# Kernel tuning notes

Measured on AMD Instinct MI355X. Metric: run time of the kernel, lower is better.

Reference implementation:

```python
import jax, jax.numpy as jnp
import numpy as np
from jax import lax

B, C, P, H = 4, 3, 160, 32          # batch of box patches, channels, patch size, score-net hidden
TEMB = 64                            # time-embedding dim
BETA0, BETA1 = 0.1, 20.0             # subVP SDE beta_min / beta_max
T_EPS = 1e-5                         # integration start time (timesteps=(1e-5, 1))
N_STEPS = 10                         # (1 - eps) / ode_step_size with step_size=0.1


def _conv(x, w, b):
    y = lax.conv_general_dilated(x, w, (1, 1), 'SAME',
                                 dimension_numbers=('NCHW', 'OIHW', 'NCHW'))
    return y + b[None, :, None, None]


def _time_emb(t):
    half = TEMB // 2
    freqs = jnp.exp(-np.log(10000.0) / (half - 1) * jnp.arange(half, dtype=jnp.float32))
    a = t[:, None] * 999.0 * freqs[None, :]   # continuous t scaled as in score_sde
    return jnp.concatenate([jnp.sin(a), jnp.cos(a)], axis=-1)


def _score_net(x, t, params):
    w1, b1, wt, bt, w2, b2, w3, b3 = params
    emb = _time_emb(t) @ wt + bt                       # [B, H]
    h = jax.nn.relu(_conv(x, w1, b1) + emb[:, :, None, None])
    h = jax.nn.relu(_conv(h, w2, b2))
    return _conv(h, w3, b3)


def _drift(x, tvec, params):
    # subVP probability-flow ODE drift: f(x,t) - 0.5 * g(t)^2 * score(x,t)
    bd = BETA1 - BETA0
    beta_t = BETA0 + tvec * bd
    lmc = -0.25 * tvec ** 2 * bd - 0.5 * tvec * BETA0   # log mean coeff
    std = 1.0 - jnp.exp(2.0 * lmc)                      # marginal std
    g2 = beta_t * (1.0 - jnp.exp(4.0 * lmc))            # diffusion^2
    score = _score_net(x, tvec, params) / std[:, None, None, None]
    return -0.5 * beta_t[:, None, None, None] * x - 0.5 * g2[:, None, None, None] * score


def _forward(patches, hs_epsilon, params):
    eps = jnp.broadcast_to(hs_epsilon, patches.shape)   # fixed Rademacher probe
    dt = (1.0 - T_EPS) / N_STEPS

    def rhs(x, t):
        tvec = jnp.ones((x.shape[0],), x.dtype) * t
        # Skilling-Hutchinson divergence: eps^T J eps via one jvp
        drift, jv = jax.jvp(lambda xx: _drift(xx, tvec, params), (x,), (eps,))
        return drift, jnp.sum(jv * eps, axis=(1, 2, 3))

    def step(carry, t0):
        x, lp = carry
        k1x, k1l = rhs(x, t0)
        k2x, k2l = rhs(x + 0.5 * dt * k1x, t0 + 0.5 * dt)
        k3x, k3l = rhs(x + 0.5 * dt * k2x, t0 + 0.5 * dt)
        k4x, k4l = rhs(x + dt * k3x, t0 + dt)
        x = x + (dt / 6.0) * (k1x + 2.0 * k2x + 2.0 * k3x + k4x)
        lp = lp + (dt / 6.0) * (k1l + 2.0 * k2l + 2.0 * k3l + k4l)
        return (x, lp), None

    ts = T_EPS + dt * jnp.arange(N_STEPS, dtype=patches.dtype)
    init = (patches, jnp.zeros((patches.shape[0],), patches.dtype))
    (z, delta_logp), _ = lax.scan(jax.checkpoint(step), init, ts)

    Ndim = float(np.prod(patches.shape[1:]))
    prior_logp = -0.5 * Ndim * np.log(2.0 * np.pi) - 0.5 * jnp.sum(z ** 2, axis=(1, 2, 3))
    bpd = -(prior_logp + delta_logp) / np.log(2.0)
    return bpd / Ndim                                   # per-patch NLL (bits/dim)


def setup_inputs() -> dict:
    key = jax.random.key(0)
    ks = jax.random.split(key, 6)
    s = 0.05
    return {
        'patches': jax.random.normal(ks[0], (B, C, P, P), jnp.float32),
        'hs_epsilon': jnp.sign(jax.random.normal(ks[1], (1, C, P, P), jnp.float32)),
        'w1': jax.random.normal(ks[2], (H, C, 3, 3), jnp.float32) * s,
        'b1': jnp.zeros((H,), jnp.float32),
        'wt': jax.random.normal(ks[3], (TEMB, H), jnp.float32) * s,
        'bt': jnp.zeros((H,), jnp.float32),
        'w2': jax.random.normal(ks[4], (H, H, 3, 3), jnp.float32) * s,
        'b2': jnp.zeros((H,), jnp.float32),
        'w3': jax.random.normal(ks[5], (C, H, 3, 3), jnp.float32) * s,
        'b3': jnp.zeros((C,), jnp.float32),
    }


def reference(patches, hs_epsilon, w1, b1, wt, bt, w2, b2, w3, b3):
    params = (w1, b1, wt, bt, w2, b2, w3, b3)
    return _forward(patches, hs_epsilon, params)
```

## Files before the change

kernel.cpp:

```cpp
#include <hip/hip_runtime.h>
#include <hip/hip_bf16.h>
#include <math.h>

#define PW 160
#define PSQ 25600
#define NB 4
#define NX 307200
#define NDIM 76800

#define TY 10
#define TX 20
#define XW 26
#define XSZ 416
#define H1W 24
#define H2W 22
#define H2N 264
#define OUTN 200

typedef __attribute__((ext_vector_type(8))) short short8;
typedef __attribute__((ext_vector_type(4))) float float4v;

struct TS40 { float t[40]; };
struct MC40 { float m[40]; float A; };

__device__ __forceinline__ short bf16s(float f) {
    return __builtin_bit_cast(short, __float2bfloat16(f));
}
__device__ __forceinline__ unsigned packbf(float a, float b) {
    return (unsigned)(unsigned short)bf16s(a) | ((unsigned)(unsigned short)bf16s(b) << 16);
}

__global__ void emb_kernel(const float* __restrict__ wt, const float* __restrict__ bt,
                           float* __restrict__ emb, TS40 ts) {
    int r = blockIdx.x, k = threadIdx.x;
    __shared__ float e64[64];
    float t = ts.t[r];
    int j = k & 31;
    float freq = expf(-0.29710775393471556f * (float)j);
    float a = t * 999.0f * freq;
    e64[k] = (k < 32) ? sinf(a) : cosf(a);
    __syncthreads();
    if (k < 32) {
        float acc = bt[k];
        #pragma unroll 8
        for (int q = 0; q < 64; q++) acc += e64[q] * wt[q * 32 + k];
        emb[r * 32 + k] = acc;
    }
}

__global__ void repack_kernel(const float* __restrict__ w1, const float* __restrict__ w2,
                              const float* __restrict__ w3, short* __restrict__ w1p,
                              short* __restrict__ w2p, short* __restrict__ w3p) {
    int tid = blockIdx.x * 256 + threadIdx.x;
    if (tid < 9216) {
        int j = tid & 7, co = (tid >> 3) & 31, q4 = tid >> 8;
        int tap = q4 >> 2, quad = q4 & 3;
        int ci = ((j >> 2) << 4) + quad * 4 + (j & 3);
        w2p[tid] = bf16s(w2[(co * 32 + ci) * 9 + tap]);
    }
    if (tid < 4608) {
        int j = tid & 7, co = (tid >> 3) & 15, q4 = tid >> 7;
        int tap = q4 >> 2, quad = q4 & 3;
        int ci = ((j >> 2) << 4) + quad * 4 + (j & 3);
        float v = (co < 3) ? w3[(co * 32 + ci) * 9 + tap] : 0.0f;
        w3p[tid] = bf16s(v);
    }
    if (tid < 1024) {
        int j = tid & 7, co = (tid >> 3) & 31, quad = tid >> 8;
        int k = quad * 8 + j;
        float v = 0.0f;
        if (k < 27) { int tap = (k * 11) >> 5; int ci = k - tap * 3; v = w1[(co * 3 + ci) * 9 + tap]; }
        w1p[tid] = bf16s(v);
    }
}

__global__ __launch_bounds__(256) void teps_conv1(
    const float* __restrict__ xin, const short* __restrict__ w1p,
    short* __restrict__ outH) {
    const int tile = blockIdx.x;
    const int ty0 = (tile / 10) * 16, tx0 = (tile % 10) * 16;
    const int tid = threadIdx.x;
    const int lane = tid & 63, wv = tid >> 6;
    const int n = lane & 15, quad = lane >> 4;
    __shared__ float sX[3 * 324];
    for (int idx = tid; idx < 3 * 324; idx += 256) {
        int ci = idx / 324, p = idx - ci * 324;
        int ly = p / 18, lx = p - ly * 18;
        int gy = ty0 + ly - 1, gx = tx0 + lx - 1;
        float v = 0.0f;
        if (gy >= 0 && gy < PW && gx >= 0 && gx < PW)
            v = xin[(size_t)ci * PSQ + gy * PW + gx];
        sX[idx] = v;
    }
    __syncthreads();
    int offj[8], valj[8];
    #pragma unroll
    for (int j = 0; j < 8; ++j) {
        int k = quad * 8 + j;
        valj[j] = (k < 27);
        int tap = (k * 11) >> 5; if (k >= 27) tap = 0;
        int ci = k - tap * 3;
        int dy = (tap * 11) >> 5, dx = tap - dy * 3;
        offj[j] = valj[j] ? (ci * 324 + dy * 18 + dx + n) : 0;
    }
    short8 a0 = *(const short8*)&w1p[(quad * 32 + n) * 8];
    short8 a1 = *(const short8*)&w1p[(quad * 32 + 16 + n) * 8];
    #pragma unroll
    for (int r = 0; r < 4; ++r) {
        int row = wv * 4 + r;
        short8 bb;
        #pragma unroll
        for (int j = 0; j < 8; ++j) {
            float v = valj[j] ? sX[offj[j] + row * 18] : 0.0f;
            bb[j] = bf16s(v);
        }
        float4v acc0 = {0.f, 0.f, 0.f, 0.f}, acc1 = {0.f, 0.f, 0.f, 0.f};
        acc0 = __builtin_amdgcn_mfma_f32_16x16x32_bf16(a0, bb, acc0, 0, 0, 0);
        acc1 = __builtin_amdgcn_mfma_f32_16x16x32_bf16(a1, bb, acc1, 0, 0, 0);
        int pix = (ty0 + row) * PW + tx0 + n;
        uint2 h0, h1v;
        h0.x = packbf(acc0[0], acc0[1]); h0.y = packbf(acc0[2], acc0[3]);
        h1v.x = packbf(acc1[0], acc1[1]); h1v.y = packbf(acc1[2], acc1[3]);
        *(uint2*)&outH[(size_t)pix * 32 + quad * 4] = h0;
        *(uint2*)&outH[(size_t)pix * 32 + 16 + quad * 4] = h1v;
    }
}

__global__ __launch_bounds__(512, 4) void fused_stage(
    const float* __restrict__ xin, float* __restrict__ x0,
    float* __restrict__ xacc, float* __restrict__ xst,
    const short* __restrict__ w1p, const short* __restrict__ w2p,
    const short* __restrict__ w3p, const float* __restrict__ b1,
    const float* __restrict__ b2, const float* __restrict__ b3,
    const float* __restrict__ embr, const short* __restrict__ tepsb,
    const float* __restrict__ epsin, float* __restrict__ Sacc,
    float c1, float c2, float dt, int mode) {
    const int bid = blockIdx.x;
    const int tile = ((bid & 7) << 4) | (bid >> 3);
    const int b = blockIdx.y;
    const int oy = (tile >> 3) * TY, ox = (tile & 7) * TX;
    const int tid = threadIdx.x;
    const int lane = tid & 63, wv = tid >> 6;
    const int n = lane & 15, quad = lane >> 4;

    __shared__ __align__(16) char smem[77104];
    short* sH1 = (short*)smem;
    short* sD1 = (short*)(smem + 21504);
    short* sH2 = (short*)(smem + 43008);
    short* sD2 = (short*)(smem + 59904);
    short* sX  = (short*)(smem + 43008);
    float* sOut = (float*)smem;
    float* sBE = (float*)(smem + 76800);
    float* sB2 = (float*)(smem + 76928);
    float* sB3 = (float*)(smem + 77056);
    float* wsum = (float*)(smem + 77072);

    uint2 pt0[3], pt1[3];
    #pragma unroll
    for (int it = 0; it < 3; ++it) {
        int t = wv + it * 8;
        int tt = (t < 21) ? t : 0;
        int p = tt * 16 + n;
        int ry = p / H1W, rx = p - ry * H1W;
        int gy = oy - 2 + ry, gx = ox - 2 + rx;
        int ok = (t < 21) && gy >= 0 && gy < PW && gx >= 0 && gx < PW;
        size_t tbase = ok ? ((size_t)(gy * PW + gx) * 32) : 0;
        pt0[it] = *(const uint2*)&tepsb[tbase + quad * 4];
        pt1[it] = *(const uint2*)&tepsb[tbase + 16 + quad * 4];
    }

    if (tid < 32) { sBE[tid] = b1[tid] + embr[tid]; sB2[tid] = b2[tid]; }
    if (tid < 3) sB3[tid] = b3[tid];

    for (int idx = tid; idx < 3 * XSZ; idx += 512) {
        int ci = idx / XSZ, p = idx - ci * XSZ;
        int ly = p / XW, lx = p - ly * XW;
        int gy = oy - 3 + ly, gx = ox - 3 + lx;
        float v = 0.0f;
        if (gy >= 0 && gy < PW && gx >= 0 && gx < PW)
            v = xin[(size_t)(b * 3 + ci) * PSQ + gy * PW + gx];
        sX[idx] = bf16s(v);
    }
    __syncthreads();

    {
        int koff[8], kval[8];
        #pragma unroll
        for (int j = 0; j < 8; ++j) {
            int k = quad * 8 + j;
            kval[j] = (k < 27);
            int tap = (k * 11) >> 5; if (k >= 27) tap = 0;
            int ci = k - tap * 3;
            int dy = (tap * 11) >> 5, dx = tap - dy * 3;
            koff[j] = kval[j] ? (ci * XSZ + dy * XW + dx) : 0;
        }
        short8 a0 = *(const short8*)&w1p[(quad * 32 + n) * 8];
        short8 a1 = *(const short8*)&w1p[(quad * 32 + 16 + n) * 8];
        #pragma unroll
        for (int it = 0; it < 3; ++it) {
            int t = wv + it * 8;
            if (t < 21) {
                int p = t * 16 + n;
                int ry = p / H1W, rx = p - ry * H1W;
                int gy = oy - 2 + ry, gx = ox - 2 + rx;
                int inimg = (gy >= 0 && gy < PW && gx >= 0 && gx < PW);
                int base = ry * XW + rx;
                short8 bb;
                #pragma unroll
                for (int j = 0; j < 8; ++j)
                    bb[j] = kval[j] ? sX[koff[j] + base] : (short)0;
                float4v acc0 = {0.f, 0.f, 0.f, 0.f}, acc1 = {0.f, 0.f, 0.f, 0.f};
                acc0 = __builtin_amdgcn_mfma_f32_16x16x32_bf16(a0, bb, acc0, 0, 0, 0);
                acc1 = __builtin_amdgcn_mfma_f32_16x16x32_bf16(a1, bb, acc1, 0, 0, 0);
                int swz = (p & 7) << 4;
                unsigned hq[4], dq[4];
                #pragma unroll
                for (int mt = 0; mt < 2; ++mt) {
                    float4v* ac = mt ? &acc1 : &acc0;
                    uint2 t2 = mt ? pt1[it] : pt0[it];
                    int co0 = mt * 16 + quad * 4;
                    unsigned ts4[4] = {t2.x & 0xFFFFu, t2.x >> 16, t2.y & 0xFFFFu, t2.y >> 16};
                    unsigned hv[4], dv[4];
                    #pragma unroll
                    for (int g = 0; g < 4; ++g) {
                        float pre = (*ac)[g] + sBE[co0 + g];
                        hv[g] = inimg ? (unsigned)(unsigned short)bf16s(fmaxf(pre, 0.0f)) : 0u;
                        dv[g] = (inimg && pre > 0.0f) ? ts4[g] : 0u;
                    }
                    hq[mt * 2]     = hv[0] | (hv[1] << 16);
                    hq[mt * 2 + 1] = hv[2] | (hv[3] << 16);
                    dq[mt * 2]     = dv[0] | (dv[1] << 16);
                    dq[mt * 2 + 1] = dv[2] | (dv[3] << 16);
                }
                int byw = ((p << 6) | (quad << 4)) ^ swz;
                uint4 H4 = {hq[0], hq[1], hq[2], hq[3]};
                uint4 D4 = {dq[0], dq[1], dq[2], dq[3]};
                *(uint4*)((char*)sH1 + byw) = H4;
                *(uint4*)((char*)sD1 + byw) = D4;
            }
        }
    }
    __syncthreads();

    {
        short8 a2[9][2];
        #pragma unroll
        for (int tap = 0; tap < 9; ++tap) {
            a2[tap][0] = *(const short8*)&w2p[((tap * 4 + quad) * 32 + n) * 8];
            a2[tap][1] = *(const short8*)&w2p[((tap * 4 + quad) * 32 + 16 + n) * 8];
        }
        for (int t = wv; t < 17; t += 8) {
            int p = t * 16 + n;
            int pc = p < H2N ? p : (H2N - 1);
            int ry = pc / H2W, rx = pc - ry * H2W;
            float4v aP0 = {0.f,0.f,0.f,0.f}, aP1 = {0.f,0.f,0.f,0.f};
            float4v aD0 = {0.f,0.f,0.f,0.f}, aD1 = {0.f,0.f,0.f,0.f};
            #pragma unroll
            for (int tap = 0; tap < 9; ++tap) {
                int dy = (tap * 11) >> 5, dx = tap - dy * 3;
                int q = (ry + dy) * H1W + rx + dx;
                int byr = ((q << 6) | (quad << 4)) ^ ((q & 7) << 4);
                short8 bp = *(const short8*)((const char*)sH1 + byr);
                short8 bd = *(const short8*)((const char*)sD1 + byr);
                aP0 = __builtin_amdgcn_mfma_f32_16x16x32_bf16(a2[tap][0], bp, aP0, 0, 0, 0);
                aP1 = __builtin_amdgcn_mfma_f32_16x16x32_bf16(a2[tap][1], bp, aP1, 0, 0, 0);
                aD0 = __builtin_amdgcn_mfma_f32_16x16x32_bf16(a2[tap][0], bd, aD0, 0, 0, 0);
                aD1 = __builtin_amdgcn_mfma_f32_16x16x32_bf16(a2[tap][1], bd, aD1, 0, 0, 0);
            }
            int gy = oy - 1 + ry, gx = ox - 1 + rx;
            int inimg = (gy >= 0 && gy < PW && gx >= 0 && gx < PW);
            if (p < H2N) {
                int swz = (p & 7) << 4;
                unsigned hq[4], dq[4];
                #pragma unroll
                for (int mt = 0; mt < 2; ++mt) {
                    float4v* acP = mt ? &aP1 : &aP0;
                    float4v* acD = mt ? &aD1 : &aD0;
                    int co0 = mt * 16 + quad * 4;
                    unsigned hv[4], dv[4];
                    #pragma unroll
                    for (int g = 0; g < 4; ++g) {
                        float pre = (*acP)[g] + sB2[co0 + g];
                        hv[g] = inimg ? (unsigned)(unsigned short)bf16s(fmaxf(pre, 0.0f)) : 0u;
                        dv[g] = (inimg && pre > 0.0f) ? (unsigned)(unsigned short)bf16s((*acD)[g]) : 0u;
                    }
                    hq[mt * 2]     = hv[0] | (hv[1] << 16);
                    hq[mt * 2 + 1] = hv[2] | (hv[3] << 16);
                    dq[mt * 2]     = dv[0] | (dv[1] << 16);
                    dq[mt * 2 + 1] = dv[2] | (dv[3] << 16);
                }
                int byw = ((p << 6) | (quad << 4)) ^ swz;
                uint4 H4 = {hq[0], hq[1], hq[2], hq[3]};
                uint4 D4 = {dq[0], dq[1], dq[2], dq[3]};
                *(uint4*)((char*)sH2 + byw) = H4;
                *(uint4*)((char*)sD2 + byw) = D4;
            }
        }
    }
    __syncthreads();

    float pf_x[2], pf_e[2], pf_a[2], pf_x0[2];
    #pragma unroll
    for (int rep = 0; rep < 2; ++rep) {
        int idx = tid + rep * 512;
        int v = (idx < 3 * OUTN);
        int idc = v ? idx : 0;
        int c = idc / OUTN, pp = idc - c * OUTN;
        int ry = pp / TX, rx = pp - ry * TX;
        int pix = (oy + ry) * PW + ox + rx;
        size_t gi = (size_t)(b * 3 + c) * PSQ + pix;
        pf_x[rep] = v ? xin[gi] : 0.0f;
        pf_e[rep] = v ? epsin[c * PSQ + pix] : 0.0f;
        pf_a[rep] = 0.0f; pf_x0[rep] = 0.0f;
        if (mode >= 1) {
            pf_a[rep] = v ? xacc[gi] : 0.0f;
            pf_x0[rep] = v ? x0[gi] : 0.0f;
        }
    }

    {
        short8 a3[9];
        #pragma unroll
        for (int tap = 0; tap < 9; ++tap)
            a3[tap] = *(const short8*)&w3p[((tap * 4 + quad) * 16 + n) * 8];
        for (int t = wv; t < 13; t += 8) {
            int p = t * 16 + n;
            int pc = p < OUTN ? p : (OUTN - 1);
            int ry = pc / TX, rx = pc - ry * TX;
            float4v aP = {0.f,0.f,0.f,0.f}, aD = {0.f,0.f,0.f,0.f};
            #pragma unroll
            for (int tap = 0; tap < 9; ++tap) {
                int dy = (tap * 11) >> 5, dx = tap - dy * 3;
                int q = (ry + dy) * H2W + rx + dx;
                int byr = ((q << 6) | (quad << 4)) ^ ((q & 7) << 4);
                short8 bp = *(const short8*)((const char*)sH2 + byr);
                short8 bd = *(const short8*)((const char*)sD2 + byr);
                aP = __builtin_amdgcn_mfma_f32_16x16x32_bf16(a3[tap], bp, aP, 0, 0, 0);
                aD = __builtin_amdgcn_mfma_f32_16x16x32_bf16(a3[tap], bd, aD, 0, 0, 0);
            }
            if (quad == 0 && p < OUTN) {
                #pragma unroll
                for (int c = 0; c < 3; ++c) {
                    sOut[c * OUTN + p] = aP[c] + sB3[c];
                    sOut[3 * OUTN + c * OUTN + p] = aD[c];
                }
            }
        }
    }
    __syncthreads();

    float s = 0.0f;
    #pragma unroll
    for (int rep = 0; rep < 2; ++rep) {
        int idx = tid + rep * 512;
        if (idx < 3 * OUTN) {
            int c = idx / OUTN, pp = idx - c * OUTN;
            int ry = pp / TX, rx = pp - ry * TX;
            int pix = (oy + ry) * PW + ox + rx;
            size_t gi = (size_t)(b * 3 + c) * PSQ + pix;
            float y = sOut[c * OUTN + pp];
            float d = sOut[3 * OUTN + c * OUTN + pp];
            float xv = pf_x[rep];
            float k = -c1 * xv - c2 * y;
            if (mode == 0) {
                xacc[gi] = k;
                xst[gi] = xv + 0.5f * dt * k;
            } else if (mode == 1) {
                xacc[gi] = pf_a[rep] + 2.0f * k;
                xst[gi] = pf_x0[rep] + 0.5f * dt * k;
            } else if (mode == 2) {
                xacc[gi] = pf_a[rep] + 2.0f * k;
                xst[gi] = pf_x0[rep] + dt * k;
            } else {
                x0[gi] = pf_x0[rep] + (dt / 6.0f) * (pf_a[rep] + k);
            }
            s += d * pf_e[rep];
        }
    }
    #pragma unroll
    for (int off = 32; off > 0; off >>= 1) s += __shfl_down(s, off);
    if (lane == 0) wsum[wv] = s;
    __syncthreads();
    if (tid == 0) {
        float tot = 0.0f;
        #pragma unroll
        for (int w = 0; w < 8; ++w) tot += wsum[w];
        atomicAdd(&Sacc[b], tot);
    }
}

__global__ void sumz2_kernel(const float* __restrict__ x0, float* __restrict__ sumz2) {
    int b = blockIdx.x, seg = blockIdx.y, tid = threadIdx.x;
    const float* p = x0 + (size_t)b * NDIM + seg * 3072;
    float s = 0.0f;
    for (int i = tid; i < 3072; i += 256) { float v = p[i]; s += v * v; }
    #pragma unroll
    for (int off = 32; off > 0; off >>= 1) s += __shfl_down(s, off);
    __shared__ float wsum[4];
    if ((tid & 63) == 0) wsum[tid >> 6] = s;
    __syncthreads();
    if (tid == 0) atomicAdd(&sumz2[b], wsum[0] + wsum[1] + wsum[2] + wsum[3]);
}

__global__ void bpd_kernel(const float* __restrict__ S, const float* __restrict__ sumz2,
                           float* __restrict__ out, MC40 mc) {
    int b = threadIdx.x;
    if (b >= NB) return;
    float lp = mc.A;
    for (int r = 0; r < 40; r++) lp -= mc.m[r] * S[r * 4 + b];
    float prior = -70574.479354f - 0.5f * sumz2[b];
    out[b] = -(prior + lp) * 1.8785164100960743e-5f;
}

extern "C" void kernel_launch(void* const* d_in, const int* in_sizes, int n_in,
                              void* d_out, int out_size, void* d_ws, size_t ws_size,
                              hipStream_t stream) {
    const float* patches = (const float*)d_in[0];
    const float* epsin = (const float*)d_in[1];
    const float* w1 = (const float*)d_in[2];
    const float* b1 = (const float*)d_in[3];
    const float* wt = (const float*)d_in[4];
    const float* bt = (const float*)d_in[5];
    const float* w2 = (const float*)d_in[6];
    const float* b2 = (const float*)d_in[7];
    const float* w3 = (const float*)d_in[8];
    const float* b3 = (const float*)d_in[9];
    float* outp = (float*)d_out;
    char* wsb = (char*)d_ws;

    float* Sbuf  = (float*)(wsb + 0);
    float* sumz2 = (float*)(wsb + 640);
    float* emb   = (float*)(wsb + 1024);
    short* w1p   = (short*)(wsb + 6144);
    short* w2p   = (short*)(wsb + 8192);
    short* w3p   = (short*)(wsb + 26624);
    short* tepsb = (short*)(wsb + 36864);
    float* x0    = (float*)(wsb + 1675264);
    float* xacc  = (float*)(wsb + 2904064);
    float* xst   = (float*)(wsb + 4132864);

    const double dt = (1.0 - 1e-5) / 10.0;
    TS40 ts; MC40 mc;
    float c1a[40], c2a[40];
    double A = 0.0;
    const double wgt[4] = {1.0, 2.0, 2.0, 1.0};
    for (int i = 0; i < 10; i++) {
        double t0 = 1e-5 + dt * i;
        double tr[4] = {t0, t0 + 0.5 * dt, t0 + 0.5 * dt, t0 + dt};
        for (int s = 0; s < 4; s++) {
            int r = i * 4 + s;
            double t = tr[s];
            double beta = 0.1 + 19.9 * t;
            double lmc = -0.25 * t * t * 19.9 - 0.05 * t;
            double stdv = 1.0 - exp(2.0 * lmc);
            double g2 = beta * (1.0 - exp(4.0 * lmc));
            double c2 = 0.5 * g2 / stdv;
            ts.t[r] = (float)t;
            c1a[r] = (float)(0.5 * beta);
            c2a[r] = (float)c2;
            double coef = dt / 6.0 * wgt[s];
            mc.m[r] = (float)(coef * c2);
            A += coef * (-0.5 * beta * (double)NDIM);
        }
    }
    mc.A = (float)A;

    hipMemsetAsync(wsb, 0, 656, stream);
    hipMemcpyAsync(x0, patches, NX * sizeof(float), hipMemcpyDeviceToDevice, stream);

    emb_kernel<<<40, 64, 0, stream>>>(wt, bt, emb, ts);
    repack_kernel<<<36, 256, 0, stream>>>(w1, w2, w3, w1p, w2p, w3p);
    teps_conv1<<<100, 256, 0, stream>>>(epsin, w1p, tepsb);

    for (int i = 0; i < 10; i++) {
        for (int s = 0; s < 4; s++) {
            int r = i * 4 + s;
            const float* xin = (s == 0) ? x0 : xst;
            fused_stage<<<dim3(128, NB), 512, 0, stream>>>(
                xin, x0, xacc, xst, w1p, w2p, w3p, b1, b2, b3,
                emb + r * 32, tepsb, epsin, Sbuf + r * 4,
                c1a[r], c2a[r], (float)dt, s);
        }
    }
    sumz2_kernel<<<dim3(NB, 25), 256, 0, stream>>>(x0, sumz2);
    bpd_kernel<<<1, 64, 0, stream>>>(Sbuf, sumz2, outp, mc);
}
```

Measured before the change: 850.0 us.

## Fuse RK epilogue into conv3 loop, drop x0 copy and merge prep kernels

The final-conv output is now consumed directly in registers for the RK update and divergence sum, which removes the shared-memory staging buffer and one block-wide barrier. The per-pixel loads of x, eps, xacc and x0 move inside the tile loop, so they happen per MFMA tile by the quad-0 lanes only. The first RK step reads the input patches directly instead of copying them into a workspace buffer. The embedding and weight-repack kernels are merged into one launch. In exchange, the global loads are now less coalesced, since only 16 lanes per wave issue them, and their latency is less hidden than with the earlier prefetch.

Result: no change. 851.6 us (+0.2%).

```diff
diff --git a/kernel.cpp b/kernel.cpp
--- a/kernel.cpp
+++ b/kernel.cpp
@@ -30,47 +30,51 @@
     return (unsigned)(unsigned short)bf16s(a) | ((unsigned)(unsigned short)bf16s(b) << 16);
 }
 
-__global__ void emb_kernel(const float* __restrict__ wt, const float* __restrict__ bt,
-                           float* __restrict__ emb, TS40 ts) {
-    int r = blockIdx.x, k = threadIdx.x;
+__global__ void prep_kernel(const float* __restrict__ w1, const float* __restrict__ w2,
+                            const float* __restrict__ w3, short* __restrict__ w1p,
+                            short* __restrict__ w2p, short* __restrict__ w3p,
+                            const float* __restrict__ wt, const float* __restrict__ bt,
+                            float* __restrict__ emb, TS40 ts) {
     __shared__ float e64[64];
-    float t = ts.t[r];
-    int j = k & 31;
-    float freq = expf(-0.29710775393471556f * (float)j);
-    float a = t * 999.0f * freq;
-    e64[k] = (k < 32) ? sinf(a) : cosf(a);
-    __syncthreads();
-    if (k < 32) {
-        float acc = bt[k];
-        #pragma unroll 8
-        for (int q = 0; q < 64; q++) acc += e64[q] * wt[q * 32 + k];
-        emb[r * 32 + k] = acc;
-    }
-}
-
-__global__ void repack_kernel(const float* __restrict__ w1, const float* __restrict__ w2,
-                              const float* __restrict__ w3, short* __restrict__ w1p,
-                              short* __restrict__ w2p, short* __restrict__ w3p) {
-    int tid = blockIdx.x * 256 + threadIdx.x;
-    if (tid < 9216) {
-        int j = tid & 7, co = (tid >> 3) & 31, q4 = tid >> 8;
-        int tap = q4 >> 2, quad = q4 & 3;
-        int ci = ((j >> 2) << 4) + quad * 4 + (j & 3);
-        w2p[tid] = bf16s(w2[(co * 32 + ci) * 9 + tap]);
-    }
-    if (tid < 4608) {
-        int j = tid & 7, co = (tid >> 3) & 15, q4 = tid >> 7;
-        int tap = q4 >> 2, quad = q4 & 3;
-        int ci = ((j >> 2) << 4) + quad * 4 + (j & 3);
-        float v = (co < 3) ? w3[(co * 32 + ci) * 9 + tap] : 0.0f;
-        w3p[tid] = bf16s(v);
-    }
-    if (tid < 1024) {
-        int j = tid & 7, co = (tid >> 3) & 31, quad = tid >> 8;
-        int k = quad * 8 + j;
-        float v = 0.0f;
-        if (k < 27) { int tap = (k * 11) >> 5; int ci = k - tap * 3; v = w1[(co * 3 + ci) * 9 + tap]; }
-        w1p[tid] = bf16s(v);
+    int blk = blockIdx.x;
+    if (blk < 36) {
+        int tid = blk * 256 + threadIdx.x;
+        if (tid < 9216) {
+            int j = tid & 7, co = (tid >> 3) & 31, q4 = tid >> 8;
+            int tap = q4 >> 2, quad = q4 & 3;
+            int ci = ((j >> 2) << 4) + quad * 4 + (j & 3);
+            w2p[tid] = bf16s(w2[(co * 32 + ci) * 9 + tap]);
+        }
+        if (tid < 4608) {
+            int j = tid & 7, co = (tid >> 3) & 15, q4 = tid >> 7;
+            int tap = q4 >> 2, quad = q4 & 3;
+            int ci = ((j >> 2) << 4) + quad * 4 + (j & 3);
+            float v = (co < 3) ? w3[(co * 32 + ci) * 9 + tap] : 0.0f;
+            w3p[tid] = bf16s(v);
+        }
+        if (tid < 1024) {
+            int j = tid & 7, co = (tid >> 3) & 31, quad = tid >> 8;
+            int k = quad * 8 + j;
+            float v = 0.0f;
+            if (k < 27) { int tap = (k * 11) >> 5; int ci = k - tap * 3; v = w1[(co * 3 + ci) * 9 + tap]; }
+            w1p[tid] = bf16s(v);
+        }
+    } else {
+        int r = blk - 36, k = threadIdx.x;
+        if (k < 64) {
+            float t = ts.t[r];
+            int j = k & 31;
+            float freq = expf(-0.29710775393471556f * (float)j);
+            float a = t * 999.0f * freq;
+            e64[k] = (k < 32) ? sinf(a) : cosf(a);
+        }
+        __syncthreads();
+        if (k < 32) {
+            float acc = bt[k];
+            #pragma unroll 8
+            for (int q = 0; q < 64; q++) acc += e64[q] * wt[q * 32 + k];
+            emb[r * 32 + k] = acc;
+        }
     }
 }
 
@@ -127,8 +131,8 @@
 }
 
 __global__ __launch_bounds__(512, 4) void fused_stage(
-    const float* __restrict__ xin, float* __restrict__ x0,
-    float* __restrict__ xacc, float* __restrict__ xst,
+    const float* __restrict__ xin, const float* __restrict__ x0r,
+    float* __restrict__ x0w, float* __restrict__ xacc, float* __restrict__ xst,
     const short* __restrict__ w1p, const short* __restrict__ w2p,
     const short* __restrict__ w3p, const float* __restrict__ b1,
     const float* __restrict__ b2, const float* __restrict__ b3,
@@ -149,7 +153,6 @@
     short* sH2 = (short*)(smem + 43008);
     short* sD2 = (short*)(smem + 59904);
     short* sX  = (short*)(smem + 43008);
-    float* sOut = (float*)smem;
     float* sBE = (float*)(smem + 76800);
     float* sB2 = (float*)(smem + 76928);
     float* sB3 = (float*)(smem + 77056);
@@ -299,25 +302,7 @@
     }
     __syncthreads();
 
-    float pf_x[2], pf_e[2], pf_a[2], pf_x0[2];
-    #pragma unroll
-    for (int rep = 0; rep < 2; ++rep) {
-        int idx = tid + rep * 512;
-        int v = (idx < 3 * OUTN);
-        int idc = v ? idx : 0;
-        int c = idc / OUTN, pp = idc - c * OUTN;
-        int ry = pp / TX, rx = pp - ry * TX;
-        int pix = (oy + ry) * PW + ox + rx;
-        size_t gi = (size_t)(b * 3 + c) * PSQ + pix;
-        pf_x[rep] = v ? xin[gi] : 0.0f;
-        pf_e[rep] = v ? epsin[c * PSQ + pix] : 0.0f;
-        pf_a[rep] = 0.0f; pf_x0[rep] = 0.0f;
-        if (mode >= 1) {
-            pf_a[rep] = v ? xacc[gi] : 0.0f;
-            pf_x0[rep] = v ? x0[gi] : 0.0f;
-        }
-    }
-
+    float s = 0.0f;
     {
         short8 a3[9];
         #pragma unroll
@@ -327,6 +312,20 @@
             int p = t * 16 + n;
             int pc = p < OUTN ? p : (OUTN - 1);
             int ry = pc / TX, rx = pc - ry * TX;
+            int act = (quad == 0 && p < OUTN);
+            int pix = (oy + ry) * PW + ox + rx;
+            float fx[3], fe[3], fa[3], f0[3];
+            #pragma unroll
+            for (int c = 0; c < 3; ++c) {
+                size_t gi = (size_t)(b * 3 + c) * PSQ + pix;
+                fx[c] = act ? xin[gi] : 0.0f;
+                fe[c] = act ? epsin[c * PSQ + pix] : 0.0f;
+                fa[c] = 0.0f; f0[c] = 0.0f;
+                if (mode >= 1) {
+                    fa[c] = act ? xacc[gi] : 0.0f;
+                    f0[c] = act ? x0r[gi] : 0.0f;
+                }
+            }
             float4v aP = {0.f,0.f,0.f,0.f}, aD = {0.f,0.f,0.f,0.f};
             #pragma unroll
             for (int tap = 0; tap < 9; ++tap) {
@@ -338,43 +337,29 @@
                 aP = __builtin_amdgcn_mfma_f32_16x16x32_bf16(a3[tap], bp, aP, 0, 0, 0);
                 aD = __builtin_amdgcn_mfma_f32_16x16x32_bf16(a3[tap], bd, aD, 0, 0, 0);
             }
-            if (quad == 0 && p < OUTN) {
+            if (act) {
                 #pragma unroll
                 for (int c = 0; c < 3; ++c) {
-                    sOut[c * OUTN + p] = aP[c] + sB3[c];
-                    sOut[3 * OUTN + c * OUTN + p] = aD[c];
+                    float y = aP[c] + sB3[c];
+                    float d = aD[c];
+                    float xv = fx[c];
+                    float k = -c1 * xv - c2 * y;
+                    size_t gi = (size_t)(b * 3 + c) * PSQ + pix;
+                    if (mode == 0) {
+                        xacc[gi] = k;
+                        xst[gi] = xv + 0.5f * dt * k;
+                    } else if (mode == 1) {
+                        xacc[gi] = fa[c] + 2.0f * k;
+                        xst[gi] = f0[c] + 0.5f * dt * k;
+                    } else if (mode == 2) {
+                        xacc[gi] = fa[c] + 2.0f * k;
+                        xst[gi] = f0[c] + dt * k;
+                    } else {
+                        x0w[gi] = f0[c] + (dt / 6.0f) * (fa[c] + k);
+                    }
+                    s += d * fe[c];
                 }
             }
-        }
-    }
-    __syncthreads();
-
-    float s = 0.0f;
-    #pragma unroll
-    for (int rep = 0; rep < 2; ++rep) {
-        int idx = tid + rep * 512;
-        if (idx < 3 * OUTN) {
-            int c = idx / OUTN, pp = idx - c * OUTN;
-            int ry = pp / TX, rx = pp - ry * TX;
-            int pix = (oy + ry) * PW + ox + rx;
-            size_t gi = (size_t)(b * 3 + c) * PSQ + pix;
-            float y = sOut[c * OUTN + pp];
-            float d = sOut[3 * OUTN + c * OUTN + pp];
-            float xv = pf_x[rep];
-            float k = -c1 * xv - c2 * y;
-            if (mode == 0) {
-                xacc[gi] = k;
-                xst[gi] = xv + 0.5f * dt * k;
-            } else if (mode == 1) {
-                xacc[gi] = pf_a[rep] + 2.0f * k;
-                xst[gi] = pf_x0[rep] + 0.5f * dt * k;
-            } else if (mode == 2) {
-                xacc[gi] = pf_a[rep] + 2.0f * k;
-                xst[gi] = pf_x0[rep] + dt * k;
-            } else {
-                x0[gi] = pf_x0[rep] + (dt / 6.0f) * (pf_a[rep] + k);
-            }
-            s += d * pf_e[rep];
         }
     }
     #pragma unroll
@@ -435,7 +420,7 @@
     short* w2p   = (short*)(wsb + 8192);
     short* w3p   = (short*)(wsb + 26624);
     short* tepsb = (short*)(wsb + 36864);
-    float* x0    = (float*)(wsb + 1675264);
+    float* x0ws  = (float*)(wsb + 1675264);
     float* xacc  = (float*)(wsb + 2904064);
     float* xst   = (float*)(wsb + 4132864);
 
@@ -466,22 +451,21 @@
     mc.A = (float)A;
 
     hipMemsetAsync(wsb, 0, 656, stream);
-    hipMemcpyAsync(x0, patches, NX * sizeof(float), hipMemcpyDeviceToDevice, stream);
-
-    emb_kernel<<<40, 64, 0, stream>>>(wt, bt, emb, ts);
-    repack_kernel<<<36, 256, 0, stream>>>(w1, w2, w3, w1p, w2p, w3p);
+
+    prep_kernel<<<76, 256, 0, stream>>>(w1, w2, w3, w1p, w2p, w3p, wt, bt, emb, ts);
     teps_conv1<<<100, 256, 0, stream>>>(epsin, w1p, tepsb);
 
     for (int i = 0; i < 10; i++) {
+        const float* x0r = (i == 0) ? patches : x0ws;
         for (int s = 0; s < 4; s++) {
             int r = i * 4 + s;
-            const float* xin = (s == 0) ? x0 : xst;
+            const float* xin = (s == 0) ? x0r : xst;
             fused_stage<<<dim3(128, NB), 512, 0, stream>>>(
-                xin, x0, xacc, xst, w1p, w2p, w3p, b1, b2, b3,
+                xin, x0r, x0ws, xacc, xst, w1p, w2p, w3p, b1, b2, b3,
                 emb + r * 32, tepsb, epsin, Sbuf + r * 4,
                 c1a[r], c2a[r], (float)dt, s);
         }
     }
-    sumz2_kernel<<<dim3(NB, 25), 256, 0, stream>>>(x0, sumz2);
+    sumz2_kernel<<<dim3(NB, 25), 256, 0, stream>>>(x0ws, sumz2);
     bpd_kernel<<<1, 64, 0, stream>>>(Sbuf, sumz2, outp, mc);
 }
```
